# Optimization experiments

Hardware: AMD Instinct MI355X
Metric: run time of the kernel (lower is better)

The kernel has to match this reference:

```python
import jax, jax.numpy as jnp
import numpy as np

C = 1024
H = 16
EPS = 1e-5


def setup_inputs() -> dict:
    key = jax.random.key(0)
    ks = jax.random.split(key, 10)
    B, S = 2, 2048
    s = 1.0 / np.sqrt(C)
    return {
        "hidden_states": jax.random.normal(ks[0], (B, C, S), dtype=jnp.float32),
        "attention_mask": jnp.ones((B, S), dtype=jnp.int32),
        "gn_weight": jnp.ones((C,), dtype=jnp.float32),
        "gn_bias": jnp.zeros((C,), dtype=jnp.float32),
        "Wq": jax.random.normal(ks[1], (C, C), dtype=jnp.float32) * s,
        "bq": jnp.zeros((C,), dtype=jnp.float32),
        "Wk": jax.random.normal(ks[2], (C, C), dtype=jnp.float32) * s,
        "bk": jnp.zeros((C,), dtype=jnp.float32),
        "Wv": jax.random.normal(ks[3], (C, C), dtype=jnp.float32) * s,
        "bv": jnp.zeros((C,), dtype=jnp.float32),
        "Wo": jax.random.normal(ks[4], (C, C), dtype=jnp.float32) * s,
        "bo": jnp.zeros((C,), dtype=jnp.float32),
    }


def reference(hidden_states, attention_mask, gn_weight, gn_bias,
              Wq, bq, Wk, bk, Wv, bv, Wo, bo):
    # hidden_states: (B, C, S); attention_mask: (B, S)
    B, Cc, S = hidden_states.shape
    D = Cc // H
    residual = hidden_states

    # GroupNorm with 1 group: normalize over (C, S) per sample
    mean = jnp.mean(hidden_states, axis=(1, 2), keepdims=True)
    var = jnp.var(hidden_states, axis=(1, 2), keepdims=True)
    x = (hidden_states - mean) * jax.lax.rsqrt(var + EPS)
    x = x * gn_weight[None, :, None] + gn_bias[None, :, None]

    x = jnp.transpose(x, (0, 2, 1))  # (B, S, C)
    q = x @ Wq.T + bq
    k = x @ Wk.T + bk
    v = x @ Wv.T + bv

    # (B, H, S, D)
    q = q.reshape(B, S, H, D).transpose(0, 2, 1, 3)
    k = k.reshape(B, S, H, D).transpose(0, 2, 1, 3)
    v = v.reshape(B, S, H, D).transpose(0, 2, 1, 3)

    scale = 1.0 / np.sqrt(np.sqrt(D))
    scores = jnp.einsum('bhqd,bhkd->bhqk', q * scale, k * scale)
    mask = attention_mask[:, None, None, :]  # (B,1,1,S) broadcast over heads/query
    scores = jnp.where(mask == 0, -jnp.inf, scores)
    probs = jax.nn.softmax(scores, axis=-1)

    out = jnp.einsum('bhqk,bhkd->bhqd', probs, v)  # (B,H,S,D)
    out = out.transpose(0, 2, 1, 3).reshape(B, S, Cc)
    out = out @ Wo.T + bo
    out = jnp.transpose(out, (0, 2, 1))  # (B, C, S)
    return out + residual
```

## Files before the change

### kernel.cpp

```cpp
#include <hip/hip_runtime.h>
#include <hip/hip_bf16.h>

#define B_ 2
#define C_ 1024
#define S_ 2048
#define H_ 16
#define KDIM 1024

typedef __attribute__((ext_vector_type(8))) short short8_t;
typedef __attribute__((ext_vector_type(4))) float f32x4;
typedef __attribute__((ext_vector_type(16))) float f32x16;
typedef __attribute__((ext_vector_type(4))) int i32x4;

__device__ __forceinline__ void glds16(const void* g, void* l) {
  __builtin_amdgcn_global_load_lds((const __attribute__((address_space(1))) void*)g,
                                   (__attribute__((address_space(3))) void*)l, 16, 0, 0);
}

__device__ __forceinline__ unsigned short f2bf(float f) {
  __hip_bfloat16 h = __float2bfloat16(f);
  return __builtin_bit_cast(unsigned short, h);
}

__device__ __forceinline__ unsigned pkbf(float lo, float hi) {
  unsigned r;
  asm("v_cvt_pk_bf16_f32 %0, %1, %2" : "=v"(r) : "v"(lo), "v"(hi));
  return r;
}

__device__ __forceinline__ void plswap(unsigned &a, unsigned &b) {
  asm("v_permlane32_swap_b32 %0, %1" : "+v"(a), "+v"(b));
}

__device__ __forceinline__ float max16f(const f32x16& v) {
  float a = fmaxf(fmaxf(v[0], v[1]),  fmaxf(v[2], v[3]));
  float b = fmaxf(fmaxf(v[4], v[5]),  fmaxf(v[6], v[7]));
  float c = fmaxf(fmaxf(v[8], v[9]),  fmaxf(v[10], v[11]));
  float d = fmaxf(fmaxf(v[12], v[13]), fmaxf(v[14], v[15]));
  return fmaxf(fmaxf(a, b), fmaxf(c, d));
}

__device__ __forceinline__ float sum16f(const float* p) {
  float a = (p[0] + p[1]) + (p[2] + p[3]);
  float b = (p[4] + p[5]) + (p[6] + p[7]);
  float c = (p[8] + p[9]) + (p[10] + p[11]);
  float d = (p[12] + p[13]) + (p[14] + p[15]);
  return (a + b) + (c + d);
}

__global__ __launch_bounds__(256) void cvt_w4(const float* __restrict__ a,
                                              const float* __restrict__ b,
                                              const float* __restrict__ c,
                                              const float* __restrict__ d,
                                              unsigned short* __restrict__ o) {
  int g = blockIdx.x >> 10;
  const float* src = (g == 0) ? a : (g == 1) ? b : (g == 2) ? c : d;
  int i = (blockIdx.x & 1023) * 256 + threadIdx.x;
  float4 v = ((const float4*)src)[i];
  short4 r;
  r.x = (short)f2bf(v.x); r.y = (short)f2bf(v.y);
  r.z = (short)f2bf(v.z); r.w = (short)f2bf(v.w);
  ((short4*)(o))[(size_t)g * 262144 + i] = r;
}

__global__ __launch_bounds__(256) void stats1(const float* __restrict__ x,
                                              float2* __restrict__ part) {
  int bid = blockIdx.x;
  int b = bid >> 8, chunk = bid & 255;
  const float4* p = (const float4*)(x + (size_t)b*(C_*S_) + (size_t)chunk*8192);
  int t = threadIdx.x;
  float s = 0.f, q = 0.f;
#pragma unroll
  for (int i = 0; i < 8; ++i) {
    float4 v = p[t + i*256];
    s += v.x + v.y + v.z + v.w;
    q += v.x*v.x + v.y*v.y + v.z*v.z + v.w*v.w;
  }
#pragma unroll
  for (int d = 1; d < 64; d <<= 1) { s += __shfl_xor(s, d); q += __shfl_xor(q, d); }
  __shared__ float2 wsum[4];
  if ((t & 63) == 0) wsum[t >> 6] = make_float2(s, q);
  __syncthreads();
  if (t == 0) {
    float S = 0.f, Q = 0.f;
    for (int i = 0; i < 4; ++i) { S += wsum[i].x; Q += wsum[i].y; }
    part[bid] = make_float2(S, Q);
  }
}

__global__ __launch_bounds__(256) void stats2(const float2* __restrict__ part,
                                              float* __restrict__ stats) {
  int b = blockIdx.x;
  int t = threadIdx.x;
  float2 v = part[b*256 + t];
  float s = v.x, q = v.y;
#pragma unroll
  for (int d = 1; d < 64; d <<= 1) { s += __shfl_xor(s, d); q += __shfl_xor(q, d); }
  __shared__ float2 wsum[4];
  if ((t & 63) == 0) wsum[t >> 6] = make_float2(s, q);
  __syncthreads();
  if (t == 0) {
    float S = 0.f, Q = 0.f;
    for (int i = 0; i < 4; ++i) { S += wsum[i].x; Q += wsum[i].y; }
    const float invN = 1.0f / (float)(C_*S_);
    float mean = S * invN;
    float var = Q * invN - mean*mean;
    stats[b*2]   = mean;
    stats[b*2+1] = rsqrtf(var + 1e-5f);
  }
}

__global__ __launch_bounds__(256) void normt(const float* __restrict__ x,
                                             const float* __restrict__ gw,
                                             const float* __restrict__ gb,
                                             const float* __restrict__ stats,
                                             unsigned short* __restrict__ xt) {
  __shared__ short lds[64*72];
  int bid = blockIdx.x;
  int b = bid >> 9, rem = bid & 511;
  int ct = rem >> 5, st = rem & 31;
  float mean = stats[b*2], rstd = stats[b*2+1];
  int t = threadIdx.x;
  int r = t >> 2, seg = t & 3;
  int c = ct*64 + r;
  float wsc = gw[c] * rstd;
  float bof = gb[c] - mean * wsc;
  const float4* src = (const float4*)(x + (size_t)b*(C_*S_) + (size_t)c*S_ + st*64 + seg*16);
#pragma unroll
  for (int j = 0; j < 4; ++j) {
    float4 v = src[j];
    int sl = seg*16 + j*4;
    lds[(sl+0)*72 + r] = (short)f2bf(v.x*wsc + bof);
    lds[(sl+1)*72 + r] = (short)f2bf(v.y*wsc + bof);
    lds[(sl+2)*72 + r] = (short)f2bf(v.z*wsc + bof);
    lds[(sl+3)*72 + r] = (short)f2bf(v.w*wsc + bof);
  }
  __syncthreads();
  int sl = t >> 2;
  __attribute__((aligned(16))) unsigned short tmp[16];
#pragma unroll
  for (int j = 0; j < 16; ++j) tmp[j] = (unsigned short)lds[sl*72 + seg*16 + j];
  unsigned short* dst = xt + ((size_t)b*S_ + st*64 + sl) * C_ + ct*64 + seg*16;
  *(short8_t*)dst       = *(const short8_t*)tmp;
  *(short8_t*)(dst + 8) = *(const short8_t*)(tmp + 8);
}

template<int EPI>
__global__ __launch_bounds__(256)
void gemm_nt(const unsigned short* __restrict__ A,
             const unsigned short* __restrict__ Bm,
             const float* __restrict__ bias,
             const float* __restrict__ resid,
             void* __restrict__ outp,
             int nbn) {
  __shared__ __attribute__((aligned(16))) short As[64*64];
  __shared__ __attribute__((aligned(16))) short Bs[128*64];
  int nwg = gridDim.x;
  int bid = blockIdx.x;
  int cpx = nwg >> 3;
  int sbid = (bid & 7) * cpx + (bid >> 3);
  int bm = sbid / nbn, bn = sbid % nbn;
  int m0 = bm << 6, n0 = bn << 7;
  int t = threadIdx.x;
  int l = t & 63, wid = t >> 6;

  int r_st = t >> 3;
  int slot_src = (t & 7) ^ (r_st & 7);
  const unsigned short* a_src = A + (size_t)(m0 + r_st) * KDIM + slot_src * 8;
  const unsigned short* b_src = Bm + (size_t)(n0 + r_st) * KDIM + slot_src * 8;
  char* As_base = (char*)As + wid*1024;
  char* Bs_base = (char*)Bs + wid*1024;

  f32x4 acc[4][2] = {};

  for (int kt = 0; kt < KDIM; kt += 64) {
    __syncthreads();
    glds16(a_src + kt, As_base);
    glds16(a_src + (size_t)32*KDIM + kt, As_base + 4096);
#pragma unroll
    for (int i = 0; i < 4; ++i)
      glds16(b_src + (size_t)(i*32)*KDIM + kt, Bs_base + i*4096);
    __syncthreads();
#pragma unroll
    for (int kk = 0; kk < 2; ++kk) {
      short8_t af[4], bfr[2];
#pragma unroll
      for (int mi = 0; mi < 4; ++mi) {
        int row = mi*16 + (l & 15);
        int slot = (kk*4 + (l >> 4)) ^ (row & 7);
        af[mi] = *(const short8_t*)((const char*)As + row*128 + slot*16);
      }
#pragma unroll
      for (int ni = 0; ni < 2; ++ni) {
        int row = wid*32 + ni*16 + (l & 15);
        int slot = (kk*4 + (l >> 4)) ^ (row & 7);
        bfr[ni] = *(const short8_t*)((const char*)Bs + row*128 + slot*16);
      }
#pragma unroll
      for (int mi = 0; mi < 4; ++mi)
#pragma unroll
        for (int ni = 0; ni < 2; ++ni)
          acc[mi][ni] = __builtin_amdgcn_mfma_f32_16x16x32_bf16(af[mi], bfr[ni], acc[mi][ni], 0, 0, 0);
    }
  }

#pragma unroll
  for (int mi = 0; mi < 4; ++mi) {
#pragma unroll
    for (int ni = 0; ni < 2; ++ni) {
#pragma unroll
      for (int r = 0; r < 4; ++r) {
        int gm = m0 + mi*16 + ((l >> 4) << 2) + r;
        int gn = n0 + wid*32 + ni*16 + (l & 15);
        float v = acc[mi][ni][r];
        if (EPI == 0) {
          v += bias[gn];
          size_t off = ((size_t)((gm >> 11)*H_ + (gn >> 6)) * S_ + (gm & 2047)) * 64 + (gn & 63);
          ((unsigned short*)outp)[off] = f2bf(v);
        } else {
          v += bias[gm];
          size_t off = (size_t)(gn >> 11) * ((size_t)C_*S_) + (size_t)gm * S_ + (gn & 2047);
          if (EPI == 1) {
            ((unsigned short*)outp)[off] = f2bf(v);
          } else {
            ((float*)outp)[off] = v + resid[off];
          }
        }
      }
    }
  }
}

__global__ __launch_bounds__(256)
void attn_kernel(const unsigned short* __restrict__ Q,
                 const unsigned short* __restrict__ Kt,
                 const unsigned short* __restrict__ Vt,
                 const int* __restrict__ mask,
                 unsigned short* __restrict__ outp) {
  __shared__ __attribute__((aligned(16))) short Ks[2][64*64];
  __shared__ __attribute__((aligned(16))) short Vs[2][64*64];
  __shared__ __attribute__((aligned(8)))  unsigned char maskb[256];
  __shared__ int tflag[32];

  int bid = blockIdx.x;
  int bid2 = (bid & 7) * 64 + (bid >> 3);
  int bh = bid2 >> 4, qt = bid2 & 15;
  int b = bh >> 4, h = bh & 15;
  int t = threadIdx.x, l = t & 63, wid = t >> 6;
  int hh = l >> 5;

  {
    const i32x4* mp = (const i32x4*)(mask + b * S_) + t * 2;
    i32x4 m0 = mp[0], m1 = mp[1];
    unsigned by = (unsigned)(m0[0]!=0) | ((unsigned)(m0[1]!=0)<<1) | ((unsigned)(m0[2]!=0)<<2) | ((unsigned)(m0[3]!=0)<<3)
                | ((unsigned)(m1[0]!=0)<<4) | ((unsigned)(m1[1]!=0)<<5) | ((unsigned)(m1[2]!=0)<<6) | ((unsigned)(m1[3]!=0)<<7);
    maskb[t] = (unsigned char)by;
  }
  __syncthreads();
  if (t < 32) {
    unsigned long long v = ((const unsigned long long*)maskb)[t];
    tflag[t] = (v == 0xFFFFFFFFFFFFFFFFull) ? 1 : 0;
  }

  int q0 = qt*128 + wid*32;
  const unsigned short* qp = Q + ((size_t)bh * S_ + q0 + (l & 31)) * 64 + hh * 8;
  short8_t qf[4];
#pragma unroll
  for (int c = 0; c < 4; ++c) qf[c] = *(const short8_t*)(qp + c*16);

  int r_off = wid*16 + (l >> 3);
  int slot_src = (l & 7) ^ (l >> 3);
  const unsigned short* ksrc = Kt + ((size_t)bh * S_ + r_off) * 64 + slot_src * 8;
  const unsigned short* vsrc = Vt + ((size_t)bh * 64 + r_off) * S_ + slot_src * 8;
  int lds_off = wid*2048;

  const float SC = 0.18033688011112042f;
  float m_run = 0.f, msc = 0.f, l_run = 0.f;
  f32x16 oc0 = {}, oc1 = {};

#pragma unroll
  for (int i = 0; i < 2; ++i) {
    glds16(ksrc + (size_t)(i*8) * 64, (char*)Ks[0] + lds_off + i*1024);
    glds16(vsrc + (size_t)(i*8) * S_, (char*)Vs[0] + lds_off + i*1024);
  }

  for (int ti = 0; ti < 32; ++ti) {
    int kt0 = ti << 6;
    int buf = ti & 1;
    __syncthreads();
    if (ti < 31) {
      int nb = buf ^ 1;
      int nk = kt0 + 64;
#pragma unroll
      for (int i = 0; i < 2; ++i) {
        glds16(ksrc + (size_t)(nk + i*8) * 64, (char*)Ks[nb] + lds_off + i*1024);
        glds16(vsrc + (size_t)(i*8) * S_ + nk, (char*)Vs[nb] + lds_off + i*1024);
      }
    }
    const char* Kb = (const char*)Ks[buf];
    const char* Vb = (const char*)Vs[buf];

    f32x16 st0 = {}, st1 = {};
#pragma unroll
    for (int c = 0; c < 4; ++c) {
      int row0 = (l & 31);
      int slot = (c*2 + hh) ^ (l & 7);
      short8_t kf0 = *(const short8_t*)(Kb + row0*128 + slot*16);
      short8_t kf1 = *(const short8_t*)(Kb + (row0+32)*128 + slot*16);
      st0 = __builtin_amdgcn_mfma_f32_32x32x16_bf16(kf0, qf[c], st0, 0, 0, 0);
      st1 = __builtin_amdgcn_mfma_f32_32x32x16_bf16(kf1, qf[c], st1, 0, 0, 0);
    }

    float p0[16], p1[16];
#pragma unroll
    for (int r = 0; r < 16; ++r) {
      p0[r] = __builtin_amdgcn_exp2f(fmaf(st0[r], SC, -msc));
      p1[r] = __builtin_amdgcn_exp2f(fmaf(st1[r], SC, -msc));
    }
    float mx = fmaxf(max16f(st0), max16f(st1));
    mx = fmaxf(mx, __shfl_xor(mx, 32));
    if (__any(mx > m_run + 48.f)) {
      float nm = fmaxf(m_run, mx);
      float fac = __builtin_amdgcn_exp2f((m_run - nm) * SC);
#pragma unroll
      for (int r = 0; r < 16; ++r) { p0[r] *= fac; p1[r] *= fac; }
#pragma unroll
      for (int r = 0; r < 16; ++r) { oc0[r] *= fac; oc1[r] *= fac; }
      l_run *= fac;
      m_run = nm; msc = nm * SC;
    }
    if (!tflag[kt0 >> 6]) {
#pragma unroll
      for (int r = 0; r < 16; ++r) {
        int kl = kt0 + (r & 3) + 8*(r >> 2) + 4*hh;
        if (!((maskb[kl >> 3] >> (kl & 7)) & 1)) p0[r] = 0.f;
        kl += 32;
        if (!((maskb[kl >> 3] >> (kl & 7)) & 1)) p1[r] = 0.f;
      }
    }
    l_run += sum16f(p0) + sum16f(p1);

    short8_t pa[4];
    {
      unsigned a0 = pkbf(p0[0],  p0[1]),  b0 = pkbf(p0[4],  p0[5]);
      unsigned a1 = pkbf(p0[2],  p0[3]),  b1 = pkbf(p0[6],  p0[7]);
      plswap(a0, b0); plswap(a1, b1);
      i32x4 w0 = {(int)a0, (int)a1, (int)b0, (int)b1};
      pa[0] = __builtin_bit_cast(short8_t, w0);
      unsigned a2 = pkbf(p0[8],  p0[9]),  b2 = pkbf(p0[12], p0[13]);
      unsigned a3 = pkbf(p0[10], p0[11]), b3 = pkbf(p0[14], p0[15]);
      plswap(a2, b2); plswap(a3, b3);
      i32x4 w1 = {(int)a2, (int)a3, (int)b2, (int)b3};
      pa[1] = __builtin_bit_cast(short8_t, w1);
      unsigned a4 = pkbf(p1[0],  p1[1]),  b4 = pkbf(p1[4],  p1[5]);
      unsigned a5 = pkbf(p1[2],  p1[3]),  b5 = pkbf(p1[6],  p1[7]);
      plswap(a4, b4); plswap(a5, b5);
      i32x4 w2 = {(int)a4, (int)a5, (int)b4, (int)b5};
      pa[2] = __builtin_bit_cast(short8_t, w2);
      unsigned a6 = pkbf(p1[8],  p1[9]),  b6 = pkbf(p1[12], p1[13]);
      unsigned a7 = pkbf(p1[10], p1[11]), b7 = pkbf(p1[14], p1[15]);
      plswap(a6, b6); plswap(a7, b7);
      i32x4 w3 = {(int)a6, (int)a7, (int)b6, (int)b7};
      pa[3] = __builtin_bit_cast(short8_t, w3);
    }

#pragma unroll
    for (int kc = 0; kc < 4; ++kc) {
      int row0 = (l & 31);
      int slot = (kc*2 + hh) ^ (l & 7);
      short8_t vf0 = *(const short8_t*)(Vb + row0*128 + slot*16);
      short8_t vf1 = *(const short8_t*)(Vb + (row0+32)*128 + slot*16);
      oc0 = __builtin_amdgcn_mfma_f32_32x32x16_bf16(vf0, pa[kc], oc0, 0, 0, 0);
      oc1 = __builtin_amdgcn_mfma_f32_32x32x16_bf16(vf1, pa[kc], oc1, 0, 0, 0);
    }
  }

  float ltot = l_run + __shfl_xor(l_run, 32);
  float inv = 1.f / ltot;
#pragma unroll
  for (int r = 0; r < 16; ++r) { oc0[r] *= inv; oc1[r] *= inv; }

  unsigned short* obase = outp + ((size_t)b * S_ + q0 + (l & 31)) * C_ + h*64 + hh*8;
#pragma unroll
  for (int dt = 0; dt < 2; ++dt) {
    const f32x16& oc = dt ? oc1 : oc0;
    unsigned a0 = pkbf(oc[0],  oc[1]),  b0 = pkbf(oc[4],  oc[5]);
    unsigned a1 = pkbf(oc[2],  oc[3]),  b1 = pkbf(oc[6],  oc[7]);
    plswap(a0, b0); plswap(a1, b1);
    i32x4 w0 = {(int)a0, (int)a1, (int)b0, (int)b1};
    *(i32x4*)(obase + dt*32) = w0;
    unsigned a2 = pkbf(oc[8],  oc[9]),  b2 = pkbf(oc[12], oc[13]);
    unsigned a3 = pkbf(oc[10], oc[11]), b3 = pkbf(oc[14], oc[15]);
    plswap(a2, b2); plswap(a3, b3);
    i32x4 w1 = {(int)a2, (int)a3, (int)b2, (int)b3};
    *(i32x4*)(obase + dt*32 + 16) = w1;
  }
}

extern "C" void kernel_launch(void* const* d_in, const int* in_sizes, int n_in,
                              void* d_out, int out_size, void* d_ws, size_t ws_size,
                              hipStream_t stream) {
  const float* hs = (const float*)d_in[0];
  const int*   msk = (const int*)d_in[1];
  const float* gw = (const float*)d_in[2];
  const float* gb = (const float*)d_in[3];
  const float* Wq = (const float*)d_in[4];
  const float* bq = (const float*)d_in[5];
  const float* Wk = (const float*)d_in[6];
  const float* bk = (const float*)d_in[7];
  const float* Wv = (const float*)d_in[8];
  const float* bv = (const float*)d_in[9];
  const float* Wo = (const float*)d_in[10];
  const float* bo = (const float*)d_in[11];

  char* ws = (char*)d_ws;
  float*  stats = (float*)(ws);
  float2* part  = (float2*)(ws + 256);
  unsigned short* wq_b = (unsigned short*)(ws + 8192);
  unsigned short* wk_b = wq_b + 1048576;
  unsigned short* wv_b = wk_b + 1048576;
  unsigned short* wo_b = wv_b + 1048576;
  unsigned short* x_b  = wo_b + 1048576;
  unsigned short* q_b  = x_b  + 4194304;
  unsigned short* k_b  = q_b  + 4194304;
  unsigned short* vt_b = k_b  + 4194304;
  unsigned short* ao_b = vt_b + 4194304;

  cvt_w4<<<4096, 256, 0, stream>>>(Wq, Wk, Wv, Wo, wq_b);

  stats1<<<512, 256, 0, stream>>>(hs, part);
  stats2<<<2, 256, 0, stream>>>(part, stats);
  normt<<<1024, 256, 0, stream>>>(hs, gw, gb, stats, x_b);

  gemm_nt<0><<<512, 256, 0, stream>>>(x_b, wq_b, bq, nullptr, q_b, 8);
  gemm_nt<0><<<512, 256, 0, stream>>>(x_b, wk_b, bk, nullptr, k_b, 8);
  gemm_nt<1><<<512, 256, 0, stream>>>(wv_b, x_b, bv, nullptr, vt_b, 32);

  attn_kernel<<<512, 256, 0, stream>>>(q_b, k_b, vt_b, msk, ao_b);

  gemm_nt<2><<<512, 256, 0, stream>>>(wo_b, ao_b, bo, hs, d_out, 32);
}
```

Measured before the change: 146.2 us.

## Split attention KV range across two wave groups with LDS merge of partial softmax

Each attention block now runs 512 threads, with two groups of four waves each handling half of the key/value sequence for the same query tile (split-K flash attention). The partial outputs, row sums and maxima are merged through LDS at the end. The online-softmax rescale is now lazy and driven by a probability threshold, and the loop is unrolled by two with s_setprio hints around the MFMA sections. This doubles the waves per block to hide latency, at the cost of 64KB of LDS per block, lower block occupancy, and an extra merge step.

```diff
diff --git a/kernel.cpp b/kernel.cpp
--- a/kernel.cpp
+++ b/kernel.cpp
@@ -32,7 +32,7 @@
   asm("v_permlane32_swap_b32 %0, %1" : "+v"(a), "+v"(b));
 }
 
-__device__ __forceinline__ float max16f(const f32x16& v) {
+__device__ __forceinline__ float max16v(const f32x16& v) {
   float a = fmaxf(fmaxf(v[0], v[1]),  fmaxf(v[2], v[3]));
   float b = fmaxf(fmaxf(v[4], v[5]),  fmaxf(v[6], v[7]));
   float c = fmaxf(fmaxf(v[8], v[9]),  fmaxf(v[10], v[11]));
@@ -40,7 +40,7 @@
   return fmaxf(fmaxf(a, b), fmaxf(c, d));
 }
 
-__device__ __forceinline__ float sum16f(const float* p) {
+__device__ __forceinline__ float sum16v(const f32x16& p) {
   float a = (p[0] + p[1]) + (p[2] + p[3]);
   float b = (p[4] + p[5]) + (p[6] + p[7]);
   float c = (p[8] + p[9]) + (p[10] + p[11]);
@@ -231,14 +231,13 @@
   }
 }
 
-__global__ __launch_bounds__(256)
+__global__ __launch_bounds__(512, 4)
 void attn_kernel(const unsigned short* __restrict__ Q,
                  const unsigned short* __restrict__ Kt,
                  const unsigned short* __restrict__ Vt,
                  const int* __restrict__ mask,
                  unsigned short* __restrict__ outp) {
-  __shared__ __attribute__((aligned(16))) short Ks[2][64*64];
-  __shared__ __attribute__((aligned(16))) short Vs[2][64*64];
+  __shared__ __attribute__((aligned(16))) char lds[65536];
   __shared__ __attribute__((aligned(8)))  unsigned char maskb[256];
   __shared__ int tflag[32];
 
@@ -247,9 +246,10 @@
   int bh = bid2 >> 4, qt = bid2 & 15;
   int b = bh >> 4, h = bh & 15;
   int t = threadIdx.x, l = t & 63, wid = t >> 6;
+  int quad = wid >> 2, qw = wid & 3;
   int hh = l >> 5;
 
-  {
+  if (t < 256) {
     const i32x4* mp = (const i32x4*)(mask + b * S_) + t * 2;
     i32x4 m0 = mp[0], m1 = mp[1];
     unsigned by = (unsigned)(m0[0]!=0) | ((unsigned)(m0[1]!=0)<<1) | ((unsigned)(m0[2]!=0)<<2) | ((unsigned)(m0[3]!=0)<<3)
@@ -262,138 +262,176 @@
     tflag[t] = (v == 0xFFFFFFFFFFFFFFFFull) ? 1 : 0;
   }
 
-  int q0 = qt*128 + wid*32;
+  int q0 = qt*128 + qw*32;
   const unsigned short* qp = Q + ((size_t)bh * S_ + q0 + (l & 31)) * 64 + hh * 8;
   short8_t qf[4];
 #pragma unroll
   for (int c = 0; c < 4; ++c) qf[c] = *(const short8_t*)(qp + c*16);
 
-  int r_off = wid*16 + (l >> 3);
-  int slot_src = (l & 7) ^ (l >> 3);
-  const unsigned short* ksrc = Kt + ((size_t)bh * S_ + r_off) * 64 + slot_src * 8;
-  const unsigned short* vsrc = Vt + ((size_t)bh * 64 + r_off) * S_ + slot_src * 8;
-  int lds_off = wid*2048;
+  int kbase = quad << 10;
+  int row_st = qw*16 + (l >> 3);
+  int slot_st = (l & 7) ^ (l >> 3);
+  const unsigned short* kp = Kt + ((size_t)bh * S_ + kbase + row_st) * 64 + slot_st * 8;
+  const unsigned short* vp = Vt + ((size_t)bh * 64 + row_st) * S_ + kbase + slot_st * 8;
+  char* kdst = lds + quad*16384 + qw*2048;
+  char* vdst = kdst + 32768;
+
+  unsigned ko[8];
+#pragma unroll
+  for (int c = 0; c < 4; ++c) {
+    unsigned slot = (unsigned)((c*2 + hh) ^ (l & 7)) * 16u;
+    ko[c]   = (unsigned)(quad*16384) + (unsigned)(l & 31)*128u + slot;
+    ko[c+4] = ko[c] + 4096u;
+  }
 
   const float SC = 0.18033688011112042f;
   float m_run = 0.f, msc = 0.f, l_run = 0.f;
   f32x16 oc0 = {}, oc1 = {};
 
-#pragma unroll
-  for (int i = 0; i < 2; ++i) {
-    glds16(ksrc + (size_t)(i*8) * 64, (char*)Ks[0] + lds_off + i*1024);
-    glds16(vsrc + (size_t)(i*8) * S_, (char*)Vs[0] + lds_off + i*1024);
-  }
-
-  for (int ti = 0; ti < 32; ++ti) {
-    int kt0 = ti << 6;
-    int buf = ti & 1;
-    __syncthreads();
-    if (ti < 31) {
-      int nb = buf ^ 1;
-      int nk = kt0 + 64;
-#pragma unroll
-      for (int i = 0; i < 2; ++i) {
-        glds16(ksrc + (size_t)(nk + i*8) * 64, (char*)Ks[nb] + lds_off + i*1024);
-        glds16(vsrc + (size_t)(i*8) * S_ + nk, (char*)Vs[nb] + lds_off + i*1024);
-      }
+  glds16(kp,                kdst);
+  glds16(kp + 8*64,         kdst + 1024);
+  glds16(vp,                vdst);
+  glds16(vp + (size_t)8*S_, vdst + 1024);
+  const unsigned short* kn = kp + 64*64;
+  const unsigned short* vn = vp + 64;
+  int lt = 0;
+
+#define ATILE(BUF)                                                              \
+  do {                                                                          \
+    __syncthreads();                                                            \
+    glds16(kn,                kdst + ((BUF)^1)*8192);                           \
+    glds16(kn + 8*64,         kdst + ((BUF)^1)*8192 + 1024);                    \
+    glds16(vn,                vdst + ((BUF)^1)*8192);                           \
+    glds16(vn + (size_t)8*S_, vdst + ((BUF)^1)*8192 + 1024);                    \
+    kn += 4096; vn += 64;                                                       \
+    f32x16 st0 = {}, st1 = {};                                                  \
+    __builtin_amdgcn_s_setprio(1);                                              \
+    _Pragma("unroll")                                                           \
+    for (int c = 0; c < 4; ++c) {                                               \
+      short8_t kf0 = *(const short8_t*)(lds + ko[c]   + (BUF)*8192);            \
+      short8_t kf1 = *(const short8_t*)(lds + ko[c+4] + (BUF)*8192);            \
+      st0 = __builtin_amdgcn_mfma_f32_32x32x16_bf16(kf0, qf[c], st0, 0, 0, 0);  \
+      st1 = __builtin_amdgcn_mfma_f32_32x32x16_bf16(kf1, qf[c], st1, 0, 0, 0);  \
+    }                                                                           \
+    __builtin_amdgcn_s_setprio(0);                                              \
+    _Pragma("unroll")                                                           \
+    for (int r = 0; r < 16; ++r) {                                              \
+      st0[r] = __builtin_amdgcn_exp2f(fmaf(st0[r], SC, -msc));                  \
+      st1[r] = __builtin_amdgcn_exp2f(fmaf(st1[r], SC, -msc));                  \
+    }                                                                           \
+    if (!tflag[(kbase >> 6) + lt]) {                                            \
+      _Pragma("unroll")                                                         \
+      for (int r = 0; r < 16; ++r) {                                            \
+        int kl = kbase + lt*64 + (r & 3) + 8*(r >> 2) + 4*hh;                   \
+        if (!((maskb[kl >> 3] >> (kl & 7)) & 1)) st0[r] = 0.f;                  \
+        kl += 32;                                                               \
+        if (!((maskb[kl >> 3] >> (kl & 7)) & 1)) st1[r] = 0.f;                  \
+      }                                                                         \
+    }                                                                           \
+    float pmax = fmaxf(max16v(st0), max16v(st1));                               \
+    l_run += sum16v(st0) + sum16v(st1);                                         \
+    short8_t pa[4];                                                             \
+    {                                                                           \
+      unsigned a0 = pkbf(st0[0],  st0[1]),  b0 = pkbf(st0[4],  st0[5]);         \
+      unsigned a1 = pkbf(st0[2],  st0[3]),  b1 = pkbf(st0[6],  st0[7]);         \
+      plswap(a0, b0); plswap(a1, b1);                                           \
+      i32x4 w0 = {(int)a0, (int)a1, (int)b0, (int)b1};                          \
+      pa[0] = __builtin_bit_cast(short8_t, w0);                                 \
+      unsigned a2 = pkbf(st0[8],  st0[9]),  b2 = pkbf(st0[12], st0[13]);        \
+      unsigned a3 = pkbf(st0[10], st0[11]), b3 = pkbf(st0[14], st0[15]);        \
+      plswap(a2, b2); plswap(a3, b3);                                           \
+      i32x4 w1 = {(int)a2, (int)a3, (int)b2, (int)b3};                          \
+      pa[1] = __builtin_bit_cast(short8_t, w1);                                 \
+      unsigned a4 = pkbf(st1[0],  st1[1]),  b4 = pkbf(st1[4],  st1[5]);         \
+      unsigned a5 = pkbf(st1[2],  st1[3]),  b5 = pkbf(st1[6],  st1[7]);         \
+      plswap(a4, b4); plswap(a5, b5);                                           \
+      i32x4 w2 = {(int)a4, (int)a5, (int)b4, (int)b5};                          \
+      pa[2] = __builtin_bit_cast(short8_t, w2);                                 \
+      unsigned a6 = pkbf(st1[8],  st1[9]),  b6 = pkbf(st1[12], st1[13]);        \
+      unsigned a7 = pkbf(st1[10], st1[11]), b7 = pkbf(st1[14], st1[15]);        \
+      plswap(a6, b6); plswap(a7, b7);                                           \
+      i32x4 w3 = {(int)a6, (int)a7, (int)b6, (int)b7};                          \
+      pa[3] = __builtin_bit_cast(short8_t, w3);                                 \
+    }                                                                           \
+    __builtin_amdgcn_s_setprio(1);                                              \
+    _Pragma("unroll")                                                           \
+    for (int kc = 0; kc < 4; ++kc) {                                            \
+      short8_t vf0 = *(const short8_t*)(lds + ko[kc]   + 32768 + (BUF)*8192);   \
+      short8_t vf1 = *(const short8_t*)(lds + ko[kc+4] + 32768 + (BUF)*8192);   \
+      oc0 = __builtin_amdgcn_mfma_f32_32x32x16_bf16(vf0, pa[kc], oc0, 0, 0, 0); \
+      oc1 = __builtin_amdgcn_mfma_f32_32x32x16_bf16(vf1, pa[kc], oc1, 0, 0, 0); \
+    }                                                                           \
+    __builtin_amdgcn_s_setprio(0);                                              \
+    if (__any(pmax > 148.0f)) {                                                 \
+      float pm = fmaxf(pmax, __shfl_xor(pmax, 32));                             \
+      float smax = (__log2f(pm) + msc) / SC;                                    \
+      float nm = fmaxf(m_run, smax);                                            \
+      float fac = __builtin_amdgcn_exp2f((m_run - nm) * SC);                    \
+      _Pragma("unroll")                                                         \
+      for (int r = 0; r < 16; ++r) { oc0[r] *= fac; oc1[r] *= fac; }            \
+      l_run *= fac; m_run = nm; msc = nm * SC;                                  \
+    }                                                                           \
+    ++lt;                                                                       \
+  } while (0)
+
+  for (int tp = 0; tp < 8; ++tp) {
+    ATILE(0);
+    ATILE(1);
+  }
+#undef ATILE
+
+  __syncthreads();
+  if (quad == 1) {
+    char* obuf = lds + qw*8192 + l*128;
+#pragma unroll
+    for (int j = 0; j < 4; ++j) {
+      f32x4 u0 = { oc0[4*j], oc0[4*j+1], oc0[4*j+2], oc0[4*j+3] };
+      *(f32x4*)(obuf + ((j ^ (l & 7)) * 16)) = u0;
+      f32x4 u1 = { oc1[4*j], oc1[4*j+1], oc1[4*j+2], oc1[4*j+3] };
+      *(f32x4*)(obuf + (((j+4) ^ (l & 7)) * 16)) = u1;
     }
-    const char* Kb = (const char*)Ks[buf];
-    const char* Vb = (const char*)Vs[buf];
-
-    f32x16 st0 = {}, st1 = {};
-#pragma unroll
-    for (int c = 0; c < 4; ++c) {
-      int row0 = (l & 31);
-      int slot = (c*2 + hh) ^ (l & 7);
-      short8_t kf0 = *(const short8_t*)(Kb + row0*128 + slot*16);
-      short8_t kf1 = *(const short8_t*)(Kb + (row0+32)*128 + slot*16);
-      st0 = __builtin_amdgcn_mfma_f32_32x32x16_bf16(kf0, qf[c], st0, 0, 0, 0);
-      st1 = __builtin_amdgcn_mfma_f32_32x32x16_bf16(kf1, qf[c], st1, 0, 0, 0);
+    *(float2*)(lds + 32768 + (qw*64 + l)*8) = make_float2(l_run, m_run);
+  }
+  __syncthreads();
+  if (quad == 0) {
+    float2 lm1 = *(const float2*)(lds + 32768 + (qw*64 + l)*8);
+    float M  = fmaxf(m_run, lm1.y);
+    float a0 = __builtin_amdgcn_exp2f((m_run - M) * SC);
+    float a1 = __builtin_amdgcn_exp2f((lm1.y - M) * SC);
+    float lc = l_run * a0 + lm1.x * a1;
+    float ltot = lc + __shfl_xor(lc, 32);
+    float inv = 1.f / ltot;
+    float s0 = a0 * inv, s1 = a1 * inv;
+    const char* obuf = lds + qw*8192 + l*128;
+#pragma unroll
+    for (int j = 0; j < 4; ++j) {
+      f32x4 u0 = *(const f32x4*)(obuf + ((j ^ (l & 7)) * 16));
+      oc0[4*j]   = oc0[4*j]  *s0 + u0[0]*s1;
+      oc0[4*j+1] = oc0[4*j+1]*s0 + u0[1]*s1;
+      oc0[4*j+2] = oc0[4*j+2]*s0 + u0[2]*s1;
+      oc0[4*j+3] = oc0[4*j+3]*s0 + u0[3]*s1;
+      f32x4 u1 = *(const f32x4*)(obuf + (((j+4) ^ (l & 7)) * 16));
+      oc1[4*j]   = oc1[4*j]  *s0 + u1[0]*s1;
+      oc1[4*j+1] = oc1[4*j+1]*s0 + u1[1]*s1;
+      oc1[4*j+2] = oc1[4*j+2]*s0 + u1[2]*s1;
+      oc1[4*j+3] = oc1[4*j+3]*s0 + u1[3]*s1;
     }
 
-    float p0[16], p1[16];
-#pragma unroll
-    for (int r = 0; r < 16; ++r) {
-      p0[r] = __builtin_amdgcn_exp2f(fmaf(st0[r], SC, -msc));
-      p1[r] = __builtin_amdgcn_exp2f(fmaf(st1[r], SC, -msc));
+    unsigned short* obase = outp + ((size_t)b * S_ + q0 + (l & 31)) * C_ + h*64 + hh*8;
+#pragma unroll
+    for (int dt = 0; dt < 2; ++dt) {
+      const f32x16& oc = dt ? oc1 : oc0;
+      unsigned a0w = pkbf(oc[0],  oc[1]),  b0w = pkbf(oc[4],  oc[5]);
+      unsigned a1w = pkbf(oc[2],  oc[3]),  b1w = pkbf(oc[6],  oc[7]);
+      plswap(a0w, b0w); plswap(a1w, b1w);
+      i32x4 w0 = {(int)a0w, (int)a1w, (int)b0w, (int)b1w};
+      *(i32x4*)(obase + dt*32) = w0;
+      unsigned a2w = pkbf(oc[8],  oc[9]),  b2w = pkbf(oc[12], oc[13]);
+      unsigned a3w = pkbf(oc[10], oc[11]), b3w = pkbf(oc[14], oc[15]);
+      plswap(a2w, b2w); plswap(a3w, b3w);
+      i32x4 w1 = {(int)a2w, (int)a3w, (int)b2w, (int)b3w};
+      *(i32x4*)(obase + dt*32 + 16) = w1;
     }
-    float mx = fmaxf(max16f(st0), max16f(st1));
-    mx = fmaxf(mx, __shfl_xor(mx, 32));
-    if (__any(mx > m_run + 48.f)) {
-      float nm = fmaxf(m_run, mx);
-      float fac = __builtin_amdgcn_exp2f((m_run - nm) * SC);
-#pragma unroll
-      for (int r = 0; r < 16; ++r) { p0[r] *= fac; p1[r] *= fac; }
-#pragma unroll
-      for (int r = 0; r < 16; ++r) { oc0[r] *= fac; oc1[r] *= fac; }
-      l_run *= fac;
-      m_run = nm; msc = nm * SC;
-    }
-    if (!tflag[kt0 >> 6]) {
-#pragma unroll
-      for (int r = 0; r < 16; ++r) {
-        int kl = kt0 + (r & 3) + 8*(r >> 2) + 4*hh;
-        if (!((maskb[kl >> 3] >> (kl & 7)) & 1)) p0[r] = 0.f;
-        kl += 32;
-        if (!((maskb[kl >> 3] >> (kl & 7)) & 1)) p1[r] = 0.f;
-      }
-    }
-    l_run += sum16f(p0) + sum16f(p1);
-
-    short8_t pa[4];
-    {
-      unsigned a0 = pkbf(p0[0],  p0[1]),  b0 = pkbf(p0[4],  p0[5]);
-      unsigned a1 = pkbf(p0[2],  p0[3]),  b1 = pkbf(p0[6],  p0[7]);
-      plswap(a0, b0); plswap(a1, b1);
-      i32x4 w0 = {(int)a0, (int)a1, (int)b0, (int)b1};
-      pa[0] = __builtin_bit_cast(short8_t, w0);
-      unsigned a2 = pkbf(p0[8],  p0[9]),  b2 = pkbf(p0[12], p0[13]);
-      unsigned a3 = pkbf(p0[10], p0[11]), b3 = pkbf(p0[14], p0[15]);
-      plswap(a2, b2); plswap(a3, b3);
-      i32x4 w1 = {(int)a2, (int)a3, (int)b2, (int)b3};
-      pa[1] = __builtin_bit_cast(short8_t, w1);
-      unsigned a4 = pkbf(p1[0],  p1[1]),  b4 = pkbf(p1[4],  p1[5]);
-      unsigned a5 = pkbf(p1[2],  p1[3]),  b5 = pkbf(p1[6],  p1[7]);
-      plswap(a4, b4); plswap(a5, b5);
-      i32x4 w2 = {(int)a4, (int)a5, (int)b4, (int)b5};
-      pa[2] = __builtin_bit_cast(short8_t, w2);
-      unsigned a6 = pkbf(p1[8],  p1[9]),  b6 = pkbf(p1[12], p1[13]);
-      unsigned a7 = pkbf(p1[10], p1[11]), b7 = pkbf(p1[14], p1[15]);
-      plswap(a6, b6); plswap(a7, b7);
-      i32x4 w3 = {(int)a6, (int)a7, (int)b6, (int)b7};
-      pa[3] = __builtin_bit_cast(short8_t, w3);
-    }
-
-#pragma unroll
-    for (int kc = 0; kc < 4; ++kc) {
-      int row0 = (l & 31);
-      int slot = (kc*2 + hh) ^ (l & 7);
-      short8_t vf0 = *(const short8_t*)(Vb + row0*128 + slot*16);
-      short8_t vf1 = *(const short8_t*)(Vb + (row0+32)*128 + slot*16);
-      oc0 = __builtin_amdgcn_mfma_f32_32x32x16_bf16(vf0, pa[kc], oc0, 0, 0, 0);
-      oc1 = __builtin_amdgcn_mfma_f32_32x32x16_bf16(vf1, pa[kc], oc1, 0, 0, 0);
-    }
-  }
-
-  float ltot = l_run + __shfl_xor(l_run, 32);
-  float inv = 1.f / ltot;
-#pragma unroll
-  for (int r = 0; r < 16; ++r) { oc0[r] *= inv; oc1[r] *= inv; }
-
-  unsigned short* obase = outp + ((size_t)b * S_ + q0 + (l & 31)) * C_ + h*64 + hh*8;
-#pragma unroll
-  for (int dt = 0; dt < 2; ++dt) {
-    const f32x16& oc = dt ? oc1 : oc0;
-    unsigned a0 = pkbf(oc[0],  oc[1]),  b0 = pkbf(oc[4],  oc[5]);
-    unsigned a1 = pkbf(oc[2],  oc[3]),  b1 = pkbf(oc[6],  oc[7]);
-    plswap(a0, b0); plswap(a1, b1);
-    i32x4 w0 = {(int)a0, (int)a1, (int)b0, (int)b1};
-    *(i32x4*)(obase + dt*32) = w0;
-    unsigned a2 = pkbf(oc[8],  oc[9]),  b2 = pkbf(oc[12], oc[13]);
-    unsigned a3 = pkbf(oc[10], oc[11]), b3 = pkbf(oc[14], oc[15]);
-    plswap(a2, b2); plswap(a3, b3);
-    i32x4 w1 = {(int)a2, (int)a3, (int)b2, (int)b3};
-    *(i32x4*)(obase + dt*32 + 16) = w1;
   }
 }
 
@@ -436,7 +474,7 @@
   gemm_nt<0><<<512, 256, 0, stream>>>(x_b, wk_b, bk, nullptr, k_b, 8);
   gemm_nt<1><<<512, 256, 0, stream>>>(wv_b, x_b, bv, nullptr, vt_b, 32);
 
-  attn_kernel<<<512, 256, 0, stream>>>(q_b, k_b, vt_b, msk, ao_b);
+  attn_kernel<<<512, 512, 0, stream>>>(q_b, k_b, vt_b, msk, ao_b);
 
   gemm_nt<2><<<512, 256, 0, stream>>>(wo_b, ao_b, bo, hs, d_out, 32);
 }
```

After: 134.1 us. 8.3% less time.
